# Performance work log

Measured on AMD Instinct MI355X. Metric: run time of the kernel, lower is better.

## Reference

```python
import jax, jax.numpy as jnp
import numpy as np

HEADS = 8
DIM_HEAD = 64
EPS = 1e-5  # nn.InstanceNorm1d default


def _inst_norm(t):
    # t: [b, h, n, d]; InstanceNorm1d(dim_head) on (b*h, n, d) input normalizes
    # over the last (L) axis per (instance, channel) = per (b, h, n) token.
    mu = jnp.mean(t, axis=-1, keepdims=True)
    var = jnp.var(t, axis=-1, keepdims=True)  # biased, matches torch eval-mode IN
    return (t - mu) / jnp.sqrt(var + EPS)


def setup_inputs() -> dict:
    key = jax.random.key(0)
    k1, k2, k3, k4 = jax.random.split(key, 4)
    b, n, dim = 4, 8192, 256
    inner = HEADS * DIM_HEAD  # 512
    x = jax.random.normal(k1, (b, n, dim), dtype=jnp.float32)
    w_qkv = jax.random.normal(k2, (dim, 3 * inner), dtype=jnp.float32) * (1.0 / DIM_HEAD)
    w_out = jax.random.normal(k3, (inner, dim), dtype=jnp.float32) * (dim ** -0.5)
    b_out = jax.random.normal(k4, (dim,), dtype=jnp.float32) * 0.01
    return {"x": x, "w_qkv": w_qkv, "w_out": w_out, "b_out": b_out}


def reference(x, w_qkv, w_out, b_out):
    b, n, dim = x.shape
    qkv = x @ w_qkv                                   # [b, n, 3*inner]
    q, k, v = jnp.split(qkv, 3, axis=-1)
    to_heads = lambda t: t.reshape(b, n, HEADS, DIM_HEAD).transpose(0, 2, 1, 3)  # b h n d
    q, k, v = to_heads(q), to_heads(k), to_heads(v)
    # Galerkin: instance-norm K and V
    k = _inst_norm(k)
    v = _inst_norm(v)
    # associative linear attention: (k^T v) then q @ dots, scaled by 1/n
    dots = jnp.einsum('bhnd,bhne->bhde', k, v)        # [b, h, d, d]
    out = jnp.einsum('bhnd,bhde->bhne', q, dots) * (1.0 / n)  # [b, h, n, d]
    out = out.transpose(0, 2, 1, 3).reshape(b, n, HEADS * DIM_HEAD)
    return out @ w_out + b_out                        # dropout p=0 (eval)
```

## Files before the change

kernel.cpp:

```cpp
#include <hip/hip_runtime.h>
#include <hip/hip_bf16.h>
#include <stdint.h>

#define HEADS 8
#define DHEAD 64
#define BATCH 4
#define SEQ   8192
#define DIM   256
#define INNER 512
#define QKVC  1536
#define ROWS  32768
#define EPS   1e-5f

typedef unsigned short u16;
typedef unsigned long long u64;
typedef __attribute__((ext_vector_type(8))) short bf16x8;
typedef __attribute__((ext_vector_type(4))) float f32x4;

#define AS1 __attribute__((address_space(1)))
#define AS3 __attribute__((address_space(3)))

__device__ __forceinline__ void async16(const void* g, void* l) {
  __builtin_amdgcn_global_load_lds((AS1 unsigned int*)g, (AS3 unsigned int*)l, 16, 0, 0);
}

__device__ __forceinline__ float bf2f(u16 u) {
  union { uint32_t i; float f; } v; v.i = ((uint32_t)u) << 16; return v.f;
}
__device__ __forceinline__ u16 f2bf(float f) {
  union { float f; uint32_t i; } v; v.f = f;
  uint32_t x = v.i;
  return (u16)((x + 0x7fffu + ((x >> 16) & 1u)) >> 16);
}

__global__ __launch_bounds__(256) void prep(const float* __restrict__ x,
                                            const float* __restrict__ w,
                                            u16* __restrict__ xb,
                                            u16* __restrict__ wqB,
                                            u16* __restrict__ wkvT,
                                            float* __restrict__ dots) {
  int bid = blockIdx.x;
  if (bid < 8192) {
    int i = (bid * 256 + threadIdx.x) * 4;
    float4 v = *(const float4*)(x + i);
    ushort4 o; o.x = f2bf(v.x); o.y = f2bf(v.y); o.z = f2bf(v.z); o.w = f2bf(v.w);
    *(ushort4*)(xb + i) = o;
  } else if (bid < 8704) {
    int id = (bid - 8192) * 256 + threadIdx.x;
    int k = id >> 9, j = id & 511;
    wqB[id] = f2bf(w[k * QKVC + j]);
  } else if (bid < 9728) {
    int id = (bid - 8704) * 256 + threadIdx.x;
    int k = id & 255;
    int r = (id >> 8) & 127;
    int h = id >> 15;
    int oc = (r < 64) ? (512 + h * 64 + r) : (1024 + h * 64 + (r - 64));
    wkvT[id] = f2bf(w[k * QKVC + oc]);
  } else {
    int i = ((bid - 9728) * 256 + threadIdx.x) * 4;
    float4 z; z.x = 0.f; z.y = 0.f; z.z = 0.f; z.w = 0.f;
    *(float4*)(dots + i) = z;
  }
}

__device__ __forceinline__ void gemm_tile(const u16* __restrict__ A, int lda,
                                          const u16* __restrict__ Bt, int ldb,
                                          int K, int row0, int col0,
                                          u16* sA, u16* sB, f32x4 acc[4][4]) {
  const int tid = threadIdx.x, lane = tid & 63, wave = tid >> 6;
  const int mr = (wave >> 1) * 64, nc = (wave & 1) * 64;
  for (int kk = 0; kk < K; kk += 64) {
#pragma unroll
    for (int it = 0; it < 4; ++it) {
      int s = it * 256 + tid;
      int r = s >> 3, c = (s & 7) << 3;
      async16(A + (size_t)(row0 + r) * lda + kk + c, sA + (it * 256 + wave * 64) * 8);
      async16(Bt + (size_t)(col0 + r) * ldb + kk + c, sB + (it * 256 + wave * 64) * 8);
    }
    __syncthreads();
#pragma unroll
    for (int ks = 0; ks < 2; ++ks) {
      bf16x8 af[4], bfr[4];
#pragma unroll
      for (int f = 0; f < 4; ++f) {
        af[f]  = *(const bf16x8*)&sA[(mr + f * 16 + (lane & 15)) * 64 + ks * 32 + (lane >> 4) * 8];
        bfr[f] = *(const bf16x8*)&sB[(nc + f * 16 + (lane & 15)) * 64 + ks * 32 + (lane >> 4) * 8];
      }
#pragma unroll
      for (int fm = 0; fm < 4; ++fm)
#pragma unroll
        for (int fn = 0; fn < 4; ++fn)
          acc[fm][fn] = __builtin_amdgcn_mfma_f32_16x16x32_bf16(af[fm], bfr[fn], acc[fm][fn], 0, 0, 0);
    }
    __syncthreads();
  }
}

__global__ __launch_bounds__(256, 4) void gemm_kv_dots(const u16* __restrict__ A,
                                                       const u16* __restrict__ wkvT,
                                                       float* __restrict__ dots) {
  __shared__ alignas(16) u16 smem[17408];
  u16* sA  = smem;
  u16* sB  = smem + 8192;
  u16* knT = smem;
  u16* vnT = smem + 8704;

  const int tid = threadIdx.x, lane = tid & 63, wave = tid >> 6;
  const int m = lane & 15, q = lane >> 4;
  const int row0 = blockIdx.x * 128;
  const int h = blockIdx.y;
  const u16* Bt = wkvT + h * 128 * 256;
  const int half = wave & 1;
  const int rowbase = (wave >> 1) * 64;

  f32x4 acc[4][4];
#pragma unroll
  for (int i = 0; i < 4; ++i)
#pragma unroll
    for (int j = 0; j < 4; ++j) acc[i][j] = (f32x4){0.f, 0.f, 0.f, 0.f};

  gemm_tile(A, DIM, Bt, DIM, DIM, row0, 0, sA, sB, acc);

  u16* dst = half ? vnT : knT;
#pragma unroll
  for (int fm = 0; fm < 4; ++fm) {
    f32x4 s  = acc[fm][0] + acc[fm][1] + acc[fm][2] + acc[fm][3];
    f32x4 s2 = (f32x4){0.f, 0.f, 0.f, 0.f};
#pragma unroll
    for (int fn = 0; fn < 4; ++fn)
#pragma unroll
      for (int r = 0; r < 4; ++r) s2[r] = fmaf(acc[fm][fn][r], acc[fm][fn][r], s2[r]);
#pragma unroll
    for (int mask = 1; mask <= 8; mask <<= 1) {
#pragma unroll
      for (int r = 0; r < 4; ++r) {
        s[r]  += __shfl_xor(s[r],  mask, 64);
        s2[r] += __shfl_xor(s2[r], mask, 64);
      }
    }
    f32x4 mu, rs;
#pragma unroll
    for (int r = 0; r < 4; ++r) {
      mu[r] = s[r] * (1.f / 64.f);
      float var = s2[r] * (1.f / 64.f) - mu[r] * mu[r];
      rs[r] = rsqrtf(var + EPS);
    }
    const int tokb = rowbase + fm * 16 + q * 4;
#pragma unroll
    for (int fn = 0; fn < 4; ++fn) {
      int d = fn * 16 + m;
      u64 pk = 0;
#pragma unroll
      for (int r = 0; r < 4; ++r) {
        u16 hv = f2bf((acc[fm][fn][r] - mu[r]) * rs[r]);
        pk |= (u64)hv << (16 * r);
      }
      *(u64*)(dst + d * 136 + tokb) = pk;
    }
  }
  __syncthreads();

  f32x4 dacc[4];
#pragma unroll
  for (int f = 0; f < 4; ++f) dacc[f] = (f32x4){0.f, 0.f, 0.f, 0.f};
#pragma unroll
  for (int ks = 0; ks < 4; ++ks) {
    bf16x8 a = *(const bf16x8*)&knT[(wave * 16 + m) * 136 + ks * 32 + q * 8];
#pragma unroll
    for (int fn = 0; fn < 4; ++fn) {
      bf16x8 bb = *(const bf16x8*)&vnT[(fn * 16 + m) * 136 + ks * 32 + q * 8];
      dacc[fn] = __builtin_amdgcn_mfma_f32_16x16x32_bf16(a, bb, dacc[fn], 0, 0, 0);
    }
  }

  const int b = blockIdx.x >> 6;
  float* dbase = dots + (size_t)(b * 8 + h) * 4096;
#pragma unroll
  for (int fn = 0; fn < 4; ++fn) {
    int e = fn * 16 + m;
#pragma unroll
    for (int r = 0; r < 4; ++r) {
      int d = wave * 16 + q * 4 + r;
      atomicAdd(dbase + d * 64 + e, dacc[fn][r]);
    }
  }
}

__global__ __launch_bounds__(256) void make_M(const float* __restrict__ dots,
                                              const float* __restrict__ wout,
                                              u16* __restrict__ Mbt) {
  __shared__ float dl[8][64];
  const int bh = blockIdx.x, b = bh >> 3, h = bh & 7;
  const int jg = blockIdx.y;
  const int c = threadIdx.x;
  for (int i = threadIdx.x; i < 512; i += 256)
    ((float*)dl)[i] = dots[(size_t)bh * 4096 + jg * 512 + i];
  __syncthreads();
  float accv[8];
#pragma unroll
  for (int jj = 0; jj < 8; ++jj) accv[jj] = 0.f;
  for (int e = 0; e < 64; ++e) {
    float w = wout[(h * 64 + e) * DIM + c];
#pragma unroll
    for (int jj = 0; jj < 8; ++jj) accv[jj] = fmaf(dl[jj][e], w, accv[jj]);
  }
  const float inv_n = 1.0f / (float)SEQ;
  u16* outp = Mbt + ((size_t)(b * 256 + c)) * 512 + h * 64 + jg * 8;
#pragma unroll
  for (int jj = 0; jj < 8; ++jj) outp[jj] = f2bf(accv[jj] * inv_n);
}

__global__ __launch_bounds__(256) void make_G(const u16* __restrict__ Mbt,
                                              const u16* __restrict__ wqB,
                                              u16* __restrict__ Gt) {
  __shared__ alignas(16) u16 sA[128 * 64];
  __shared__ alignas(16) u16 sB[128 * 64];
  const int lane = threadIdx.x & 63, wave = threadIdx.x >> 6;
  const int row0 = blockIdx.x * 128, col0 = blockIdx.y * 128;
  const int b = blockIdx.z;
  f32x4 acc[4][4];
#pragma unroll
  for (int i = 0; i < 4; ++i)
#pragma unroll
    for (int j = 0; j < 4; ++j) acc[i][j] = (f32x4){0.f, 0.f, 0.f, 0.f};

  gemm_tile(Mbt + (size_t)b * 256 * 512, INNER, wqB, INNER, INNER, row0, col0, sA, sB, acc);

  u16* out = Gt + (size_t)b * 256 * 256;
  const int mr = (wave >> 1) * 64, nc = (wave & 1) * 64;
#pragma unroll
  for (int fm = 0; fm < 4; ++fm) {
    int rbase = row0 + mr + fm * 16 + (lane >> 4) * 4;
#pragma unroll
    for (int fn = 0; fn < 4; ++fn) {
      int col = col0 + nc + fn * 16 + (lane & 15);
#pragma unroll
      for (int r = 0; r < 4; ++r)
        out[(size_t)(rbase + r) * DIM + col] = f2bf(acc[fm][fn][r]);
    }
  }
}

__global__ __launch_bounds__(256) void gemm_out(const u16* __restrict__ A,
                                                const u16* __restrict__ Gt,
                                                const float* __restrict__ bias,
                                                float* __restrict__ out) {
  __shared__ alignas(16) u16 sA[128 * 64];
  __shared__ alignas(16) u16 sB[128 * 64];
  const int lane = threadIdx.x & 63, wave = threadIdx.x >> 6;
  const int row0 = blockIdx.x * 128, col0 = blockIdx.y * 128;
  const int b = blockIdx.x >> 6;
  const u16* Bt = Gt + (size_t)b * 256 * 256;
  f32x4 acc[4][4];
#pragma unroll
  for (int i = 0; i < 4; ++i)
#pragma unroll
    for (int j = 0; j < 4; ++j) acc[i][j] = (f32x4){0.f, 0.f, 0.f, 0.f};

  gemm_tile(A, DIM, Bt, DIM, DIM, row0, col0, sA, sB, acc);

  const int mr = (wave >> 1) * 64, nc = (wave & 1) * 64;
#pragma unroll
  for (int fm = 0; fm < 4; ++fm) {
    int rbase = row0 + mr + fm * 16 + (lane >> 4) * 4;
#pragma unroll
    for (int fn = 0; fn < 4; ++fn) {
      int col = col0 + nc + fn * 16 + (lane & 15);
      float bb = bias[col];
#pragma unroll
      for (int r = 0; r < 4; ++r)
        out[(size_t)(rbase + r) * DIM + col] = acc[fm][fn][r] + bb;
    }
  }
}

extern "C" void kernel_launch(void* const* d_in, const int* in_sizes, int n_in,
                              void* d_out, int out_size, void* d_ws, size_t ws_size,
                              hipStream_t stream) {
  const float* x     = (const float*)d_in[0];
  const float* w_qkv = (const float*)d_in[1];
  const float* w_out = (const float*)d_in[2];
  const float* b_out = (const float*)d_in[3];
  float* out = (float*)d_out;

  char* ws = (char*)d_ws;
  size_t off = 0;
  u16* xb    = (u16*)(ws + off); off += (size_t)ROWS * DIM * 2;
  u16* wqB   = (u16*)(ws + off); off += (size_t)DIM * INNER * 2;
  u16* wkvT  = (u16*)(ws + off); off += (size_t)HEADS * 128 * DIM * 2;
  float* dots = (float*)(ws + off); off += (size_t)32 * 64 * 64 * 4;
  u16* Mbt   = (u16*)(ws + off); off += (size_t)BATCH * 256 * 512 * 2;
  u16* Gt    = (u16*)(ws + off); off += (size_t)BATCH * 256 * 256 * 2;

  prep<<<9856, 256, 0, stream>>>(x, w_qkv, xb, wqB, wkvT, dots);
  gemm_kv_dots<<<dim3(ROWS / 128, HEADS), 256, 0, stream>>>(xb, wkvT, dots);
  make_M<<<dim3(32, 8), 256, 0, stream>>>(dots, w_out, Mbt);
  make_G<<<dim3(2, 2, BATCH), 256, 0, stream>>>(Mbt, wqB, Gt);
  gemm_out<<<dim3(ROWS / 128, 2), 256, 0, stream>>>(xb, Gt, b_out, out);
}
```

Baseline: 177.8 us.

## Swizzle LDS tiles and preload prepacked KV weights directly into registers

The shared GEMM tile loader now uses an XOR swizzle on the 16-byte chunk index, for both the global-to-LDS copies and the fragment reads, to cut LDS bank conflicts. The KV weight matrix is prepacked in prep into MFMA fragment order, so gemm_kv_dots loads B fragments straight from global memory into registers and skips staging them through LDS. The trade-off is higher register pressure, which the launch bound acknowledges by dropping from 4 to 3 blocks per CU. The swizzle also applies to gemm_out through gemm_tile.

```diff
diff --git a/kernel.cpp b/kernel.cpp
--- a/kernel.cpp
+++ b/kernel.cpp
@@ -37,7 +37,7 @@
                                             const float* __restrict__ w,
                                             u16* __restrict__ xb,
                                             u16* __restrict__ wqB,
-                                            u16* __restrict__ wkvT,
+                                            u16* __restrict__ wkvP,
                                             float* __restrict__ dots) {
   int bid = blockIdx.x;
   if (bid < 8192) {
@@ -51,11 +51,18 @@
     wqB[id] = f2bf(w[k * QKVC + j]);
   } else if (bid < 9728) {
     int id = (bid - 8704) * 256 + threadIdx.x;
-    int k = id & 255;
-    int r = (id >> 8) & 127;
-    int h = id >> 15;
-    int oc = (r < 64) ? (512 + h * 64 + r) : (1024 + h * 64 + (r - 64));
-    wkvT[id] = f2bf(w[k * QKVC + oc]);
+    int j    = id & 7;
+    int lane = (id >> 3) & 63;
+    int frag = (id >> 9) & 63;
+    int h    = id >> 15;
+    int fn   = frag & 3;
+    int half = (frag >> 2) & 1;
+    int ks   = (frag >> 3) & 1;
+    int kk   = frag >> 4;
+    int col  = half * 64 + fn * 16 + (lane & 15);
+    int kidx = kk * 64 + ks * 32 + (lane >> 4) * 8 + j;
+    int oc   = (col < 64) ? (512 + h * 64 + col) : (1024 + h * 64 + (col - 64));
+    wkvP[id] = f2bf(w[kidx * QKVC + oc]);
   } else {
     int i = ((bid - 9728) * 256 + threadIdx.x) * 4;
     float4 z; z.x = 0.f; z.y = 0.f; z.z = 0.f; z.w = 0.f;
@@ -68,14 +75,15 @@
                                           int K, int row0, int col0,
                                           u16* sA, u16* sB, f32x4 acc[4][4]) {
   const int tid = threadIdx.x, lane = tid & 63, wave = tid >> 6;
+  const int m = lane & 15, q = lane >> 4;
   const int mr = (wave >> 1) * 64, nc = (wave & 1) * 64;
   for (int kk = 0; kk < K; kk += 64) {
 #pragma unroll
     for (int it = 0; it < 4; ++it) {
-      int s = it * 256 + tid;
-      int r = s >> 3, c = (s & 7) << 3;
-      async16(A + (size_t)(row0 + r) * lda + kk + c, sA + (it * 256 + wave * 64) * 8);
-      async16(Bt + (size_t)(col0 + r) * ldb + kk + c, sB + (it * 256 + wave * 64) * 8);
+      int c = it * 256 + tid;
+      int r = c >> 3, kc = (c ^ r) & 7;
+      async16(A + (size_t)(row0 + r) * lda + kk + kc * 8, sA + (it * 256 + wave * 64) * 8);
+      async16(Bt + (size_t)(col0 + r) * ldb + kk + kc * 8, sB + (it * 256 + wave * 64) * 8);
     }
     __syncthreads();
 #pragma unroll
@@ -83,8 +91,10 @@
       bf16x8 af[4], bfr[4];
 #pragma unroll
       for (int f = 0; f < 4; ++f) {
-        af[f]  = *(const bf16x8*)&sA[(mr + f * 16 + (lane & 15)) * 64 + ks * 32 + (lane >> 4) * 8];
-        bfr[f] = *(const bf16x8*)&sB[(nc + f * 16 + (lane & 15)) * 64 + ks * 32 + (lane >> 4) * 8];
+        int ra = mr + f * 16 + m;
+        int rb = nc + f * 16 + m;
+        af[f]  = *(const bf16x8*)&sA[ra * 64 + (((ks * 4 + q) ^ (m & 7)) * 8)];
+        bfr[f] = *(const bf16x8*)&sB[rb * 64 + (((ks * 4 + q) ^ (m & 7)) * 8)];
       }
 #pragma unroll
       for (int fm = 0; fm < 4; ++fm)
@@ -96,12 +106,11 @@
   }
 }
 
-__global__ __launch_bounds__(256, 4) void gemm_kv_dots(const u16* __restrict__ A,
-                                                       const u16* __restrict__ wkvT,
+__global__ __launch_bounds__(256, 3) void gemm_kv_dots(const u16* __restrict__ A,
+                                                       const u16* __restrict__ wkvP,
                                                        float* __restrict__ dots) {
   __shared__ alignas(16) u16 smem[17408];
   u16* sA  = smem;
-  u16* sB  = smem + 8192;
   u16* knT = smem;
   u16* vnT = smem + 8704;
 
@@ -109,9 +118,9 @@
   const int m = lane & 15, q = lane >> 4;
   const int row0 = blockIdx.x * 128;
   const int h = blockIdx.y;
-  const u16* Bt = wkvT + h * 128 * 256;
   const int half = wave & 1;
   const int rowbase = (wave >> 1) * 64;
+  const u16* bp = wkvP + (size_t)h * 32768 + lane * 8;
 
   f32x4 acc[4][4];
 #pragma unroll
@@ -119,7 +128,37 @@
 #pragma unroll
     for (int j = 0; j < 4; ++j) acc[i][j] = (f32x4){0.f, 0.f, 0.f, 0.f};
 
-  gemm_tile(A, DIM, Bt, DIM, DIM, row0, 0, sA, sB, acc);
+#pragma unroll
+  for (int kk = 0; kk < 4; ++kk) {
+    bf16x8 breg[2][4];
+#pragma unroll
+    for (int ks = 0; ks < 2; ++ks)
+#pragma unroll
+      for (int fn = 0; fn < 4; ++fn)
+        breg[ks][fn] = *(const bf16x8*)(bp + (size_t)((((kk * 2 + ks) * 2 + half) * 4 + fn) * 512));
+#pragma unroll
+    for (int it = 0; it < 4; ++it) {
+      int c = it * 256 + tid;
+      int r = c >> 3, kc = (c ^ r) & 7;
+      async16(A + (size_t)(row0 + r) * DIM + kk * 64 + kc * 8, sA + (it * 256 + wave * 64) * 8);
+    }
+    __syncthreads();
+#pragma unroll
+    for (int ks = 0; ks < 2; ++ks) {
+      bf16x8 af[4];
+#pragma unroll
+      for (int f = 0; f < 4; ++f) {
+        int r = rowbase + f * 16 + m;
+        af[f] = *(const bf16x8*)&sA[r * 64 + (((ks * 4 + q) ^ (m & 7)) * 8)];
+      }
+#pragma unroll
+      for (int fm = 0; fm < 4; ++fm)
+#pragma unroll
+        for (int fn = 0; fn < 4; ++fn)
+          acc[fm][fn] = __builtin_amdgcn_mfma_f32_16x16x32_bf16(af[fm], breg[ks][fn], acc[fm][fn], 0, 0, 0);
+    }
+    __syncthreads();
+  }
 
   u16* dst = half ? vnT : knT;
 #pragma unroll
@@ -287,13 +326,13 @@
   size_t off = 0;
   u16* xb    = (u16*)(ws + off); off += (size_t)ROWS * DIM * 2;
   u16* wqB   = (u16*)(ws + off); off += (size_t)DIM * INNER * 2;
-  u16* wkvT  = (u16*)(ws + off); off += (size_t)HEADS * 128 * DIM * 2;
+  u16* wkvP  = (u16*)(ws + off); off += (size_t)HEADS * 128 * DIM * 2;
   float* dots = (float*)(ws + off); off += (size_t)32 * 64 * 64 * 4;
   u16* Mbt   = (u16*)(ws + off); off += (size_t)BATCH * 256 * 512 * 2;
   u16* Gt    = (u16*)(ws + off); off += (size_t)BATCH * 256 * 256 * 2;
 
-  prep<<<9856, 256, 0, stream>>>(x, w_qkv, xb, wqB, wkvT, dots);
-  gemm_kv_dots<<<dim3(ROWS / 128, HEADS), 256, 0, stream>>>(xb, wkvT, dots);
+  prep<<<9856, 256, 0, stream>>>(x, w_qkv, xb, wqB, wkvP, dots);
+  gemm_kv_dots<<<dim3(ROWS / 128, HEADS), 256, 0, stream>>>(xb, wkvP, dots);
   make_M<<<dim3(32, 8), 256, 0, stream>>>(dots, w_out, Mbt);
   make_G<<<dim3(2, 2, BATCH), 256, 0, stream>>>(Mbt, wqB, Gt);
   gemm_out<<<dim3(ROWS / 128, 2), 256, 0, stream>>>(xb, Gt, b_out, out);
```

Measured after the change: 174.2 us. 1.02x faster.
